# Optimization experiments

Measured on AMD Instinct MI355X. Metric: run time of the kernel, lower is better.

## Reference

```python
import jax, jax.numpy as jnp
import numpy as np

N = 100000
NFEAT = 128
NHID = 128
NCLASS = 40
E = 1600000
EPS = 1e-5


def _spmm(vals, src, dst, x, n):
    # y[dst] += vals * x[src]  (sparse adj @ x)
    return jax.ops.segment_sum(vals[:, None] * x[src], dst, num_segments=n)


def _bn(h, gamma, beta, rmean, rvar):
    # BatchNorm1d in eval mode (running statistics)
    return (h - rmean) * jax.lax.rsqrt(rvar + EPS) * gamma + beta


def setup_inputs() -> dict:
    key = jax.random.key(0)
    ks = jax.random.split(key, 24)
    inp = {
        'x': jax.random.normal(ks[0], (N, NFEAT), dtype=jnp.float32),
        'M': jax.random.uniform(ks[1], (N, 1), dtype=jnp.float32),
        'AM': jax.random.uniform(ks[2], (N, 1), dtype=jnp.float32),
        'srcZ': jax.random.randint(ks[3], (E,), 0, N, dtype=jnp.int32),
        'dstZ': jax.random.randint(ks[4], (E,), 0, N, dtype=jnp.int32),
        'valsZ': jax.random.uniform(ks[5], (E,), dtype=jnp.float32),
        'src': jax.random.randint(ks[6], (E,), 0, N, dtype=jnp.int32),
        'dst': jax.random.randint(ks[7], (E,), 0, N, dtype=jnp.int32),
        'vals': jax.random.uniform(ks[8], (E,), dtype=jnp.float32),
        # layer 0 (PaGConv) params
        'W0': jax.random.normal(ks[9], (NHID, NFEAT), dtype=jnp.float32) * (1.414 / np.sqrt(NFEAT)),
        'b0': jnp.zeros((NHID,), dtype=jnp.float32),
        'g0': jnp.ones((NHID,), dtype=jnp.float32),
        'be0': jnp.zeros((NHID,), dtype=jnp.float32),
        'rm0': jax.random.normal(ks[10], (NHID,), dtype=jnp.float32) * 0.1,
        'rv0': jax.random.uniform(ks[11], (NHID,), dtype=jnp.float32) + 0.5,
        # layer 1 (GConv) params
        'W1': jax.random.normal(ks[12], (NHID, NHID), dtype=jnp.float32) * (1.414 / np.sqrt(NHID)),
        'b1': jnp.zeros((NHID,), dtype=jnp.float32),
        'g1': jnp.ones((NHID,), dtype=jnp.float32),
        'be1': jnp.zeros((NHID,), dtype=jnp.float32),
        'rm1': jax.random.normal(ks[13], (NHID,), dtype=jnp.float32) * 0.1,
        'rv1': jax.random.uniform(ks[14], (NHID,), dtype=jnp.float32) + 0.5,
        # layer 2 (GConv) params
        'W2': jax.random.normal(ks[15], (NCLASS, NHID), dtype=jnp.float32) * (1.414 / np.sqrt(NHID)),
        'b2': jnp.zeros((NCLASS,), dtype=jnp.float32),
    }
    return inp


def reference(x, M, AM, srcZ, dstZ, valsZ, src, dst, vals,
              W0, b0, g0, be0, rm0, rv0,
              W1, b1, g1, be1, rm1, rv1,
              W2, b2):
    n = x.shape[0]
    # layer 0: PaGConv with adjZ: fc(spmm(adjZ, M*x) * AM), then BN + ReLU (dropout off in eval)
    h = _spmm(valsZ, srcZ, dstZ, M * x, n) * AM
    h = h @ W0.T + b0
    h = jax.nn.relu(_bn(h, g0, be0, rm0, rv0))
    # layer 1: GConv with adj: fc(spmm(adj, h)), then BN + ReLU
    h = _spmm(vals, src, dst, h, n)
    h = h @ W1.T + b1
    h = jax.nn.relu(_bn(h, g1, be1, rm1, rv1))
    # layer 2: GConv, then log_softmax
    h = _spmm(vals, src, dst, h, n)
    h = h @ W2.T + b2
    return jax.nn.log_softmax(h, axis=-1)
```

## Files before the change

kernel.cpp:

```cpp
#include <hip/hip_runtime.h>
#include <math.h>

#define NFEAT 128
#define NCLS 40
#define NCLSP 64
#define BINROWS 64
#define NBINMAX 1600
#define NBLKC 256
#define CHUNKMAX 6400
#define SEGC 7
#define RSMAX 2048

typedef short bf16x8 __attribute__((ext_vector_type(8)));
typedef float f32x4 __attribute__((ext_vector_type(4)));

__device__ __forceinline__ float bf2f(unsigned int lo16) {
  return __uint_as_float((lo16 & 0xffffu) << 16);
}
__device__ __forceinline__ unsigned int f2bf(float x) {
  unsigned int u = __float_as_uint(x);
  return (u + 0x7fffu + ((u >> 16) & 1u)) >> 16;
}

__global__ __launch_bounds__(256) void prep_all(
    const float* b0, const float* g0, const float* be0,
    const float* rm0, const float* rv0,
    const float* b1, const float* g1, const float* be1,
    const float* rm1, const float* rv1,
    float* sc0, float* sh0, float* sc1, float* sh1,
    const float* __restrict__ W0, const float* __restrict__ W1,
    const float* __restrict__ W2,
    unsigned short* __restrict__ Wb0, unsigned short* __restrict__ Wb1,
    unsigned short* __restrict__ W2hi, unsigned short* __restrict__ W2lo,
    const float* __restrict__ x, const float* __restrict__ Mv,
    unsigned short* __restrict__ xm, int n) {
  int t = threadIdx.x;
  if (blockIdx.x == 0) {
    if (t < 128) {
      float s = g0[t] * rsqrtf(rv0[t] + 1e-5f);
      sc0[t] = s;
      sh0[t] = (b0[t] - rm0[t]) * s + be0[t];
    } else {
      int i = t - 128;
      float s = g1[i] * rsqrtf(rv1[i] + 1e-5f);
      sc1[i] = s;
      sh1[i] = (b1[i] - rm1[i]) * s + be1[i];
    }
    return;
  }
  if (blockIdx.x <= 20) {
    int i = (blockIdx.x - 1) * 256 + t;
    if (i < 4096) {
      const float* W = (i < 2048) ? W0 : W1;
      unsigned short* Wb = (i < 2048) ? Wb0 : Wb1;
      int j = (i < 2048) ? i : i - 2048;
      const float4* p = (const float4*)(W + (size_t)j * 8);
      float4 v0 = p[0], v1 = p[1];
      unsigned int o0 = f2bf(v0.x) | (f2bf(v0.y) << 16);
      unsigned int o1 = f2bf(v0.z) | (f2bf(v0.w) << 16);
      unsigned int o2 = f2bf(v1.x) | (f2bf(v1.y) << 16);
      unsigned int o3 = f2bf(v1.z) | (f2bf(v1.w) << 16);
      ((uint4*)Wb)[j] = make_uint4(o0, o1, o2, o3);
    } else {
      int j = i - 4096;
      int r = j >> 4;
      float v[8] = {0.f, 0.f, 0.f, 0.f, 0.f, 0.f, 0.f, 0.f};
      if (r < NCLS) {
        const float4* p = (const float4*)(W2 + (size_t)j * 8);
        float4 a = p[0], b = p[1];
        v[0] = a.x; v[1] = a.y; v[2] = a.z; v[3] = a.w;
        v[4] = b.x; v[5] = b.y; v[6] = b.z; v[7] = b.w;
      }
      unsigned int h[8], l[8];
#pragma unroll
      for (int q = 0; q < 8; ++q) {
        h[q] = f2bf(v[q]);
        l[q] = f2bf(v[q] - bf2f(h[q]));
      }
      ((uint4*)W2hi)[j] = make_uint4(h[0] | (h[1] << 16), h[2] | (h[3] << 16),
                                     h[4] | (h[5] << 16), h[6] | (h[7] << 16));
      ((uint4*)W2lo)[j] = make_uint4(l[0] | (l[1] << 16), l[2] | (l[3] << 16),
                                     l[4] | (l[5] << 16), l[6] | (l[7] << 16));
    }
    return;
  }
  int i = (blockIdx.x - 21) * 256 + t;
  if (i >= n * (NFEAT / 8)) return;
  int row = i >> 4;
  float m = Mv[row];
  const float4* p = (const float4*)(x + (size_t)i * 8);
  float4 v0 = p[0], v1 = p[1];
  unsigned int o0 = f2bf(v0.x * m) | (f2bf(v0.y * m) << 16);
  unsigned int o1 = f2bf(v0.z * m) | (f2bf(v0.w * m) << 16);
  unsigned int o2 = f2bf(v1.x * m) | (f2bf(v1.y * m) << 16);
  unsigned int o3 = f2bf(v1.z * m) | (f2bf(v1.w * m) << 16);
  ((uint4*)xm)[i] = make_uint4(o0, o1, o2, o3);
}

__global__ __launch_bounds__(256) void bin_sort2(
    const int* __restrict__ srcZ, const int* __restrict__ dstZ, const float* __restrict__ valZ,
    const int* __restrict__ srcA, const int* __restrict__ dstA, const float* __restrict__ valA,
    int2* __restrict__ DrmZ, int2* __restrict__ DrmA,
    int2* __restrict__ binsCZ, int2* __restrict__ binsCA,
    int E, int nbin, int chunk) {
  __shared__ int2 stage[CHUNKMAX];
  __shared__ int cur[NBINMAX];
  __shared__ int ps[256];
  const int t = threadIdx.x;
  int k = blockIdx.x;
  const int* srcp; const int* dstp; const float* valp; int2* Drm; int2* binsC;
  if (k < NBLKC) {
    srcp = srcZ; dstp = dstZ; valp = valZ; Drm = DrmZ; binsC = binsCZ;
  } else {
    k -= NBLKC;
    srcp = srcA; dstp = dstA; valp = valA; Drm = DrmA; binsC = binsCA;
  }
  for (int i = t; i < nbin; i += 256) cur[i] = 0;
  __syncthreads();
  const int e0 = k * chunk, e1 = min(E, e0 + chunk);
#pragma unroll 4
  for (int e = e0 + t; e < e1; e += 256) atomicAdd(&cur[dstp[e] >> 6], 1);
  __syncthreads();
  int loc[SEGC], cnt[SEGC];
  int s = 0;
#pragma unroll
  for (int j = 0; j < SEGC; ++j) {
    int i = t * SEGC + j;
    int v = (i < nbin) ? cur[i] : 0;
    loc[j] = s; cnt[j] = v;
    s += v;
  }
  ps[t] = s;
  __syncthreads();
  for (int o = 1; o < 256; o <<= 1) {
    int x = (t >= o) ? ps[t - o] : 0;
    __syncthreads();
    ps[t] += x;
    __syncthreads();
  }
  int ex = ps[t] - s;
#pragma unroll
  for (int j = 0; j < SEGC; ++j) {
    int i = t * SEGC + j;
    if (i < nbin) {
      int o = ex + loc[j];
      Drm[(size_t)k * nbin + i] = make_int2(e0 + o, cnt[j]);
      cur[i] = o;
    }
  }
  __syncthreads();
#pragma unroll 2
  for (int e = e0 + t; e < e1; e += 256) {
    int d = dstp[e];
    int p = atomicAdd(&cur[d >> 6], 1);
    stage[p] = make_int2(srcp[e] | ((d & 63) << 17), __float_as_int(valp[e]));
  }
  __syncthreads();
  const int n = e1 - e0;
  for (int i = t; i < n; i += 256) binsC[e0 + i] = stage[i];
}

__global__ __launch_bounds__(256) void transposeD2(
    const int2* __restrict__ DrmZ, const int2* __restrict__ DrmA,
    int2* __restrict__ DbmZ, int2* __restrict__ DbmA, int nbin, int tdb) {
  __shared__ int2 st[8][256];
  int t = threadIdx.x;
  int b = blockIdx.x;
  const int2* Drm; int2* Dbm;
  if (b < tdb) {
    Drm = DrmZ; Dbm = DbmZ;
  } else {
    b -= tdb;
    Drm = DrmA; Dbm = DbmA;
  }
  int i0 = b * 8;
#pragma unroll
  for (int j = 0; j < 8; ++j) {
    int i = i0 + j;
    st[j][t] = (i < nbin) ? Drm[(size_t)t * nbin + i] : make_int2(0, 0);
  }
  __syncthreads();
  {
    int j = t >> 5, ks = (t & 31) * 8;
    int i = i0 + j;
    if (i < nbin) {
      int2* q = &Dbm[(size_t)i * NBLKC + ks];
#pragma unroll
      for (int m = 0; m < 8; ++m) q[m] = st[j][ks + m];
    }
  }
}

__global__ __launch_bounds__(256) void row_sort2(
    const int2* __restrict__ DbmZ, const int2* __restrict__ DbmA,
    const int2* __restrict__ binsCZ, const int2* __restrict__ binsCA,
    int2* __restrict__ bins2Z, int2* __restrict__ bins2A,
    int2* __restrict__ rdZ, int2* __restrict__ rdA, int n, int nbin) {
  __shared__ int2 stage[RSMAX];
  __shared__ int ps[256];
  __shared__ int rcnt[BINROWS];
  __shared__ int roff[BINROWS];
  int b = blockIdx.x;
  const int t = threadIdx.x;
  const int2* Dbm; const int2* binsC; int2* bins2; int2* rowdesc;
  if (b < nbin) {
    Dbm = DbmZ; binsC = binsCZ; bins2 = bins2Z; rowdesc = rdZ;
  } else {
    b -= nbin;
    Dbm = DbmA; binsC = binsCA; bins2 = bins2A; rowdesc = rdA;
  }
  if (t < BINROWS) rcnt[t] = 0;
  int2 run = Dbm[(size_t)b * NBLKC + t];
  ps[t] = run.y;
  __syncthreads();
  for (int o = 1; o < 256; o <<= 1) {
    int x = (t >= o) ? ps[t - o] : 0;
    __syncthreads();
    ps[t] += x;
    __syncthreads();
  }
  int mystart = ps[t] - run.y;
  for (int j = 0; j < run.y; ++j) {
    int2 en = binsC[run.x + j];
    int idx = mystart + j;
    if (idx < RSMAX) stage[idx] = en;
    atomicAdd(&rcnt[(en.x >> 17) & 63], 1);
  }
  __syncthreads();
  const int bs = b * RSMAX;
  if (t < BINROWS) {
    int c = rcnt[t];
    int s = c;
#pragma unroll
    for (int o = 1; o < 64; o <<= 1) {
      int v = __shfl_up(s, o);
      if (t >= o) s += v;
    }
    int excl = s - c;
    int row = b * BINROWS + t;
    if (row < n) rowdesc[row] = make_int2(bs + excl, c);
    roff[t] = excl;
  }
  __syncthreads();
  int total = min(ps[255], RSMAX);
  for (int i = t; i < total; i += 256) {
    int2 en = stage[i];
    int row = (en.x >> 17) & 63;
    int p = atomicAdd(&roff[row], 1);
    bins2[bs + p] = en;
  }
}

template <bool SCALE>
__global__ __launch_bounds__(256) void spmm128_sorted(
    const int2* __restrict__ rowdesc, const int2* __restrict__ bins2,
    const unsigned short* __restrict__ X, const float* __restrict__ AM,
    unsigned short* __restrict__ Y, int n) {
  int row = (blockIdx.x * 256 + threadIdx.x) >> 6;
  int lane = threadIdx.x & 63;
  if (row >= n) return;
  int2 rd = rowdesc[row];
  int s = rd.x, d = rd.y;
  int half = lane >> 5, l32 = lane & 31;
  float s0 = 0.f, s1 = 0.f, s2 = 0.f, s3 = 0.f;
  for (int kb = 0; kb < d; kb += 64) {
    int rem = min(64, d - kb);
    int2 my = (lane < rem) ? bins2[s + kb + lane] : make_int2(0, 0);
    int myc = my.x & 0x1FFFF;
    float myw = __int_as_float(my.y);
    for (int k = 0; k < rem; k += 8) {
#pragma unroll
      for (int st = 0; st < 4; ++st) {
        int idx = k + 2 * st + half;
        int c = __shfl(myc, idx);
        float wv = __shfl(myw, idx);
        uint2 pv = *(const uint2*)(X + (size_t)c * NFEAT + l32 * 4);
        s0 += wv * bf2f(pv.x);
        s1 += wv * bf2f(pv.x >> 16);
        s2 += wv * bf2f(pv.y);
        s3 += wv * bf2f(pv.y >> 16);
      }
    }
  }
  s0 += __shfl_xor(s0, 32); s1 += __shfl_xor(s1, 32);
  s2 += __shfl_xor(s2, 32); s3 += __shfl_xor(s3, 32);
  if (SCALE) {
    float am = AM[row];
    s0 *= am; s1 *= am; s2 *= am; s3 *= am;
  }
  unsigned int pk = half ? (f2bf(s2) | (f2bf(s3) << 16)) : (f2bf(s0) | (f2bf(s1) << 16));
  ((unsigned int*)Y)[(size_t)row * (NFEAT / 2) + l32 * 2 + half] = pk;
}

template <bool FUSE_G2>
__global__ __launch_bounds__(256) void gemm_mfma128(
    const unsigned short* __restrict__ Y, const unsigned short* __restrict__ Wb,
    const float* __restrict__ scale, const float* __restrict__ shift,
    unsigned short* __restrict__ Out,
    const unsigned short* __restrict__ Whi, const unsigned short* __restrict__ Wlo,
    unsigned short* __restrict__ G2, int M) {
  const int wave = threadIdx.x >> 6;
  const int lane = threadIdx.x & 63;
  const int quad = lane >> 4;
  const int l16 = lane & 15;
  const int arow = blockIdx.x * 64 + wave * 16 + l16;
  const bool rv = arow < M;

  f32x4 acc[8];
#pragma unroll
  for (int c = 0; c < 8; ++c) acc[c] = (f32x4){0.f, 0.f, 0.f, 0.f};

#pragma unroll
  for (int kc = 0; kc < 128; kc += 32) {
    bf16x8 a = rv ? *(const bf16x8*)(Y + (size_t)arow * 128 + kc + quad * 8)
                  : (bf16x8){0, 0, 0, 0, 0, 0, 0, 0};
#pragma unroll
    for (int c = 0; c < 8; ++c) {
      bf16x8 b = *(const bf16x8*)(Wb + (size_t)(c * 16 + l16) * 128 + kc + quad * 8);
      acc[c] = __builtin_amdgcn_mfma_f32_16x16x32_bf16(a, b, acc[c], 0, 0, 0);
    }
  }

  const int orow0 = blockIdx.x * 64 + wave * 16 + quad * 4;

  if constexpr (!FUSE_G2) {
#pragma unroll
    for (int c = 0; c < 8; ++c) {
      int col = c * 16 + l16;
      float sc = scale[col], sh = shift[col];
#pragma unroll
      for (int r = 0; r < 4; ++r) {
        int orow = orow0 + r;
        if (orow < M) {
          float v = fmaxf(acc[c][r] * sc + sh, 0.f);
          Out[(size_t)orow * 128 + col] = (unsigned short)f2bf(v);
        }
      }
    }
  } else {
    __shared__ unsigned short Ht[64][136];
    const int lrow0 = wave * 16 + quad * 4;
#pragma unroll
    for (int c = 0; c < 8; ++c) {
      int col = c * 16 + l16;
      float sc = scale[col], sh = shift[col];
#pragma unroll
      for (int r = 0; r < 4; ++r) {
        float v = fmaxf(acc[c][r] * sc + sh, 0.f);
        Ht[lrow0 + r][col] = (unsigned short)f2bf(v);
      }
    }
    __syncthreads();
    bf16x8 af[4];
#pragma unroll
    for (int kc = 0; kc < 4; ++kc)
      af[kc] = *(const bf16x8*)(&Ht[wave * 16 + l16][kc * 32 + quad * 8]);
    f32x4 acc2[4];
#pragma unroll
    for (int c2 = 0; c2 < 4; ++c2) acc2[c2] = (f32x4){0.f, 0.f, 0.f, 0.f};
#pragma unroll
    for (int kc = 0; kc < 4; ++kc) {
#pragma unroll
      for (int c2 = 0; c2 < 4; ++c2) {
        bf16x8 bh = *(const bf16x8*)(Whi + (size_t)(c2 * 16 + l16) * 128 + kc * 32 + quad * 8);
        bf16x8 bl = *(const bf16x8*)(Wlo + (size_t)(c2 * 16 + l16) * 128 + kc * 32 + quad * 8);
        acc2[c2] = __builtin_amdgcn_mfma_f32_16x16x32_bf16(af[kc], bh, acc2[c2], 0, 0, 0);
        acc2[c2] = __builtin_amdgcn_mfma_f32_16x16x32_bf16(af[kc], bl, acc2[c2], 0, 0, 0);
      }
    }
#pragma unroll
    for (int c2 = 0; c2 < 4; ++c2) {
      int col = c2 * 16 + l16;
#pragma unroll
      for (int r = 0; r < 4; ++r) {
        int orow = orow0 + r;
        if (orow < M) G2[(size_t)orow * NCLSP + col] = (unsigned short)f2bf(acc2[c2][r]);
      }
    }
  }
}

__global__ __launch_bounds__(256) void spmm_softmax64(
    const int2* __restrict__ rowdesc, const int2* __restrict__ bins2,
    const unsigned short* __restrict__ G2, const float* __restrict__ b2,
    float* __restrict__ out, int n) {
  int row = (blockIdx.x * 256 + threadIdx.x) >> 6;
  int lane = threadIdx.x & 63;
  if (row >= n) return;
  const int eidx = lane >> 4, q = lane & 15;
  const bool vq = q < (NCLS / 4);
  float4 bv = vq ? *(const float4*)(b2 + q * 4) : make_float4(0.f, 0.f, 0.f, 0.f);

  int2 rdv = rowdesc[row];
  int s0i = rdv.x, d = rdv.y;
  float a0 = 0.f, a1 = 0.f, a2 = 0.f, a3 = 0.f;
  for (int kb = 0; kb < d; kb += 64) {
    int rem = min(64, d - kb);
    int2 my = (lane < rem) ? bins2[s0i + kb + lane] : make_int2(0, 0);
    int myc = my.x & 0x1FFFF;
    float myw = __int_as_float(my.y);
    int steps = (rem + 3) >> 2;
#pragma unroll 4
    for (int st = 0; st < steps; ++st) {
      int idx = st * 4 + eidx;
      int c = __shfl(myc, idx);
      float wv = __shfl(myw, idx);
      uint2 pv = *(const uint2*)(G2 + (size_t)c * NCLSP + q * 4);
      a0 += wv * bf2f(pv.x);
      a1 += wv * bf2f(pv.x >> 16);
      a2 += wv * bf2f(pv.y);
      a3 += wv * bf2f(pv.y >> 16);
    }
  }
  a0 += __shfl_xor(a0, 16); a1 += __shfl_xor(a1, 16);
  a2 += __shfl_xor(a2, 16); a3 += __shfl_xor(a3, 16);
  a0 += __shfl_xor(a0, 32); a1 += __shfl_xor(a1, 32);
  a2 += __shfl_xor(a2, 32); a3 += __shfl_xor(a3, 32);
  float z0 = a0 + bv.x, z1 = a1 + bv.y, z2 = a2 + bv.z, z3 = a3 + bv.w;
  bool par = (eidx == 0) && vq;
  float m = par ? fmaxf(fmaxf(z0, z1), fmaxf(z2, z3)) : -INFINITY;
#pragma unroll
  for (int o = 1; o < 64; o <<= 1) m = fmaxf(m, __shfl_xor(m, o));
  float ex = par ? (__expf(z0 - m) + __expf(z1 - m) + __expf(z2 - m) + __expf(z3 - m)) : 0.f;
#pragma unroll
  for (int o = 1; o < 64; o <<= 1) ex += __shfl_xor(ex, o);
  float lg = m + __logf(ex);
  if (par) {
    *(float4*)&out[(size_t)row * NCLS + q * 4] =
        make_float4(z0 - lg, z1 - lg, z2 - lg, z3 - lg);
  }
}


extern "C" void kernel_launch(void* const* d_in, const int* in_sizes, int n_in,
                              void* d_out, int out_size, void* d_ws, size_t ws_size,
                              hipStream_t stream) {
  const float* x    = (const float*)d_in[0];
  const float* Mv   = (const float*)d_in[1];
  const float* AM   = (const float*)d_in[2];
  const int* srcZ   = (const int*)d_in[3];
  const int* dstZ   = (const int*)d_in[4];
  const float* valsZ= (const float*)d_in[5];
  const int* src    = (const int*)d_in[6];
  const int* dst    = (const int*)d_in[7];
  const float* vals = (const float*)d_in[8];
  const float* W0   = (const float*)d_in[9];
  const float* b0   = (const float*)d_in[10];
  const float* g0   = (const float*)d_in[11];
  const float* be0  = (const float*)d_in[12];
  const float* rm0  = (const float*)d_in[13];
  const float* rv0  = (const float*)d_in[14];
  const float* W1   = (const float*)d_in[15];
  const float* b1   = (const float*)d_in[16];
  const float* g1   = (const float*)d_in[17];
  const float* be1  = (const float*)d_in[18];
  const float* rm1  = (const float*)d_in[19];
  const float* rv1  = (const float*)d_in[20];
  const float* W2   = (const float*)d_in[21];
  const float* b2   = (const float*)d_in[22];
  float* out = (float*)d_out;

  const int N = in_sizes[1];
  const int E = in_sizes[3];
  const int NBIN = (N + BINROWS - 1) / BINROWS;
  const int CHUNK = (E + NBLKC - 1) / NBLKC;

  char* w = (char*)d_ws;
  size_t off = 0;
  auto alloc = [&](size_t bytes) -> void* {
    void* p = w + off;
    off = (off + bytes + 255) & ~(size_t)255;
    return p;
  };
  const size_t bins2Bytes = (size_t)NBIN * RSMAX * 8;
  const size_t bufBytes = (size_t)N * NFEAT * 2;
  int2* binsCZ = (int2*)alloc((size_t)NBLKC * CHUNK * 8);
  int2* binsCA = (int2*)alloc((size_t)NBLKC * CHUNK * 8);
  int2* bins2A = (int2*)alloc(bins2Bytes);
  int2* rdZ = (int2*)alloc((size_t)N * 8);
  int2* rdA = (int2*)alloc((size_t)N * 8);
  unsigned short* xm = (unsigned short*)alloc(bufBytes);
  unsigned short* bufA = (unsigned short*)alloc(bufBytes);
  unsigned short* bufB = (unsigned short*)alloc(bins2Bytes > bufBytes ? bins2Bytes : bufBytes);
  float* sc0 = (float*)alloc(128 * 4);
  float* sh0 = (float*)alloc(128 * 4);
  float* sc1 = (float*)alloc(128 * 4);
  float* sh1 = (float*)alloc(128 * 4);
  unsigned short* Wb0 = (unsigned short*)alloc(128 * 128 * 2);
  unsigned short* Wb1 = (unsigned short*)alloc(128 * 128 * 2);
  unsigned short* W2hi = (unsigned short*)alloc(64 * 128 * 2);
  unsigned short* W2lo = (unsigned short*)alloc(64 * 128 * 2);
  const size_t drmBytes = (size_t)NBLKC * NBIN * 8;
  int2* DrmZ = (int2*)((char*)bufA + 0 * drmBytes);
  int2* DrmA = (int2*)((char*)bufA + 1 * drmBytes);
  int2* DbmZ = (int2*)((char*)bufA + 2 * drmBytes);
  int2* DbmA = (int2*)((char*)bufA + 3 * drmBytes);
  int2* bins2Z = (int2*)bufB;
  unsigned short* G2 = bufB;

  const int RB = (N + 3) / 4;
  const int GB64 = (N + 63) / 64;
  const int TDB = (NBIN + 7) / 8;
  const int CONVB = (N * (NFEAT / 8) + 255) / 256;

  prep_all<<<21 + CONVB, 256, 0, stream>>>(b0, g0, be0, rm0, rv0, b1, g1, be1, rm1, rv1,
                                           sc0, sh0, sc1, sh1, W0, W1, W2,
                                           Wb0, Wb1, W2hi, W2lo, x, Mv, xm, N);

  bin_sort2<<<2 * NBLKC, 256, 0, stream>>>(srcZ, dstZ, valsZ, src, dst, vals,
                                           DrmZ, DrmA, binsCZ, binsCA, E, NBIN, CHUNK);
  transposeD2<<<2 * TDB, 256, 0, stream>>>(DrmZ, DrmA, DbmZ, DbmA, NBIN, TDB);
  row_sort2<<<2 * NBIN, 256, 0, stream>>>(DbmZ, DbmA, binsCZ, binsCA,
                                          bins2Z, bins2A, rdZ, rdA, N, NBIN);

  spmm128_sorted<true><<<RB, 256, 0, stream>>>(rdZ, bins2Z, xm, AM, bufA, N);
  gemm_mfma128<false><<<GB64, 256, 0, stream>>>(bufA, Wb0, sc0, sh0, bufB,
                                                nullptr, nullptr, nullptr, N);

  spmm128_sorted<false><<<RB, 256, 0, stream>>>(rdA, bins2A, bufB,
                                                (const float*)nullptr, bufA, N);
  gemm_mfma128<true><<<GB64, 256, 0, stream>>>(bufA, Wb1, sc1, sh1, nullptr,
                                               W2hi, W2lo, G2, N);

  spmm_softmax64<<<RB, 256, 0, stream>>>(rdA, bins2A, G2, b2, out, N);
}
```

Baseline: 510.8 us.

## Fuse sparse aggregation with the dense MFMA GEMM per layer

The separate SpMM and GEMM kernels for layers 0 and 1 are merged into one kernel. Each wave gathers 16 rows serially into a shared-memory tile and then runs the MFMA GEMM on that tile directly. This removes the write and re-read of the N×128 bf16 intermediate in global memory, along with two kernel launches. The cost is fewer waves in total, and each wave walks its rows one after another, which may reduce the memory-level parallelism of the latency-bound gather. The G2 output buffer is moved to the freed xm buffer.

Result: slower. 533.1 us (+4.4%).

```diff
diff --git a/kernel.cpp b/kernel.cpp
--- a/kernel.cpp
+++ b/kernel.cpp
@@ -251,79 +251,73 @@
   }
 }
 
-template <bool SCALE>
-__global__ __launch_bounds__(256) void spmm128_sorted(
+template <bool LAYER0>
+__global__ __launch_bounds__(128) void spmm_gemm128(
     const int2* __restrict__ rowdesc, const int2* __restrict__ bins2,
     const unsigned short* __restrict__ X, const float* __restrict__ AM,
-    unsigned short* __restrict__ Y, int n) {
-  int row = (blockIdx.x * 256 + threadIdx.x) >> 6;
-  int lane = threadIdx.x & 63;
-  if (row >= n) return;
-  int2 rd = rowdesc[row];
-  int s = rd.x, d = rd.y;
-  int half = lane >> 5, l32 = lane & 31;
-  float s0 = 0.f, s1 = 0.f, s2 = 0.f, s3 = 0.f;
-  for (int kb = 0; kb < d; kb += 64) {
-    int rem = min(64, d - kb);
-    int2 my = (lane < rem) ? bins2[s + kb + lane] : make_int2(0, 0);
-    int myc = my.x & 0x1FFFF;
-    float myw = __int_as_float(my.y);
-    for (int k = 0; k < rem; k += 8) {
-#pragma unroll
-      for (int st = 0; st < 4; ++st) {
-        int idx = k + 2 * st + half;
-        int c = __shfl(myc, idx);
-        float wv = __shfl(myw, idx);
-        uint2 pv = *(const uint2*)(X + (size_t)c * NFEAT + l32 * 4);
-        s0 += wv * bf2f(pv.x);
-        s1 += wv * bf2f(pv.x >> 16);
-        s2 += wv * bf2f(pv.y);
-        s3 += wv * bf2f(pv.y >> 16);
-      }
-    }
-  }
-  s0 += __shfl_xor(s0, 32); s1 += __shfl_xor(s1, 32);
-  s2 += __shfl_xor(s2, 32); s3 += __shfl_xor(s3, 32);
-  if (SCALE) {
-    float am = AM[row];
-    s0 *= am; s1 *= am; s2 *= am; s3 *= am;
-  }
-  unsigned int pk = half ? (f2bf(s2) | (f2bf(s3) << 16)) : (f2bf(s0) | (f2bf(s1) << 16));
-  ((unsigned int*)Y)[(size_t)row * (NFEAT / 2) + l32 * 2 + half] = pk;
-}
-
-template <bool FUSE_G2>
-__global__ __launch_bounds__(256) void gemm_mfma128(
-    const unsigned short* __restrict__ Y, const unsigned short* __restrict__ Wb,
+    const unsigned short* __restrict__ Wb,
     const float* __restrict__ scale, const float* __restrict__ shift,
-    unsigned short* __restrict__ Out,
     const unsigned short* __restrict__ Whi, const unsigned short* __restrict__ Wlo,
-    unsigned short* __restrict__ G2, int M) {
+    unsigned short* __restrict__ Out, int n) {
+  __shared__ unsigned short Yt[32][136];
   const int wave = threadIdx.x >> 6;
   const int lane = threadIdx.x & 63;
-  const int quad = lane >> 4;
-  const int l16 = lane & 15;
-  const int arow = blockIdx.x * 64 + wave * 16 + l16;
-  const bool rv = arow < M;
-
+  const int half = lane >> 5, l32 = lane & 31;
+  const int r0 = blockIdx.x * 32 + wave * 16;
+
+#pragma unroll 1
+  for (int j = 0; j < 16; ++j) {
+    int row = r0 + j;
+    float s0 = 0.f, s1 = 0.f, s2 = 0.f, s3 = 0.f;
+    if (row < n) {
+      int2 rd = rowdesc[row];
+      int s = rd.x, d = rd.y;
+      for (int kb = 0; kb < d; kb += 64) {
+        int rem = min(64, d - kb);
+        int2 my = (lane < rem) ? bins2[s + kb + lane] : make_int2(0, 0);
+        int myc = my.x & 0x1FFFF;
+        float myw = __int_as_float(my.y);
+        for (int k = 0; k < rem; k += 8) {
+#pragma unroll
+          for (int st = 0; st < 4; ++st) {
+            int idx = k + 2 * st + half;
+            int c = __shfl(myc, idx);
+            float wv = __shfl(myw, idx);
+            uint2 pv = *(const uint2*)(X + (size_t)c * NFEAT + l32 * 4);
+            s0 += wv * bf2f(pv.x);
+            s1 += wv * bf2f(pv.x >> 16);
+            s2 += wv * bf2f(pv.y);
+            s3 += wv * bf2f(pv.y >> 16);
+          }
+        }
+      }
+      s0 += __shfl_xor(s0, 32); s1 += __shfl_xor(s1, 32);
+      s2 += __shfl_xor(s2, 32); s3 += __shfl_xor(s3, 32);
+      if (LAYER0) {
+        float am = AM[row];
+        s0 *= am; s1 *= am; s2 *= am; s3 *= am;
+      }
+    }
+    unsigned int pk = half ? (f2bf(s2) | (f2bf(s3) << 16)) : (f2bf(s0) | (f2bf(s1) << 16));
+    *(unsigned int*)&Yt[wave * 16 + j][(l32 * 2 + half) * 2] = pk;
+  }
+
+  const int quad = lane >> 4, l16 = lane & 15;
+  const int orow0 = r0 + quad * 4;
   f32x4 acc[8];
 #pragma unroll
   for (int c = 0; c < 8; ++c) acc[c] = (f32x4){0.f, 0.f, 0.f, 0.f};
-
-#pragma unroll
-  for (int kc = 0; kc < 128; kc += 32) {
-    bf16x8 a = rv ? *(const bf16x8*)(Y + (size_t)arow * 128 + kc + quad * 8)
-                  : (bf16x8){0, 0, 0, 0, 0, 0, 0, 0};
+#pragma unroll
+  for (int kc = 0; kc < 4; ++kc) {
+    bf16x8 a = *(const bf16x8*)&Yt[wave * 16 + l16][kc * 32 + quad * 8];
 #pragma unroll
     for (int c = 0; c < 8; ++c) {
-      bf16x8 b = *(const bf16x8*)(Wb + (size_t)(c * 16 + l16) * 128 + kc + quad * 8);
+      bf16x8 b = *(const bf16x8*)(Wb + (size_t)(c * 16 + l16) * 128 + kc * 32 + quad * 8);
       acc[c] = __builtin_amdgcn_mfma_f32_16x16x32_bf16(a, b, acc[c], 0, 0, 0);
     }
   }
 
-  const int orow0 = blockIdx.x * 64 + wave * 16 + quad * 4;
-
-  if constexpr (!FUSE_G2) {
+  if constexpr (LAYER0) {
 #pragma unroll
     for (int c = 0; c < 8; ++c) {
       int col = c * 16 + l16;
@@ -331,15 +325,13 @@
 #pragma unroll
       for (int r = 0; r < 4; ++r) {
         int orow = orow0 + r;
-        if (orow < M) {
+        if (orow < n) {
           float v = fmaxf(acc[c][r] * sc + sh, 0.f);
           Out[(size_t)orow * 128 + col] = (unsigned short)f2bf(v);
         }
       }
     }
   } else {
-    __shared__ unsigned short Ht[64][136];
-    const int lrow0 = wave * 16 + quad * 4;
 #pragma unroll
     for (int c = 0; c < 8; ++c) {
       int col = c * 16 + l16;
@@ -347,25 +339,21 @@
 #pragma unroll
       for (int r = 0; r < 4; ++r) {
         float v = fmaxf(acc[c][r] * sc + sh, 0.f);
-        Ht[lrow0 + r][col] = (unsigned short)f2bf(v);
-      }
-    }
-    __syncthreads();
-    bf16x8 af[4];
-#pragma unroll
-    for (int kc = 0; kc < 4; ++kc)
-      af[kc] = *(const bf16x8*)(&Ht[wave * 16 + l16][kc * 32 + quad * 8]);
+        Yt[wave * 16 + quad * 4 + r][col] = (unsigned short)f2bf(v);
+      }
+    }
     f32x4 acc2[4];
 #pragma unroll
     for (int c2 = 0; c2 < 4; ++c2) acc2[c2] = (f32x4){0.f, 0.f, 0.f, 0.f};
 #pragma unroll
     for (int kc = 0; kc < 4; ++kc) {
+      bf16x8 hf = *(const bf16x8*)&Yt[wave * 16 + l16][kc * 32 + quad * 8];
 #pragma unroll
       for (int c2 = 0; c2 < 4; ++c2) {
         bf16x8 bh = *(const bf16x8*)(Whi + (size_t)(c2 * 16 + l16) * 128 + kc * 32 + quad * 8);
         bf16x8 bl = *(const bf16x8*)(Wlo + (size_t)(c2 * 16 + l16) * 128 + kc * 32 + quad * 8);
-        acc2[c2] = __builtin_amdgcn_mfma_f32_16x16x32_bf16(af[kc], bh, acc2[c2], 0, 0, 0);
-        acc2[c2] = __builtin_amdgcn_mfma_f32_16x16x32_bf16(af[kc], bl, acc2[c2], 0, 0, 0);
+        acc2[c2] = __builtin_amdgcn_mfma_f32_16x16x32_bf16(hf, bh, acc2[c2], 0, 0, 0);
+        acc2[c2] = __builtin_amdgcn_mfma_f32_16x16x32_bf16(hf, bl, acc2[c2], 0, 0, 0);
       }
     }
 #pragma unroll
@@ -374,7 +362,7 @@
 #pragma unroll
       for (int r = 0; r < 4; ++r) {
         int orow = orow0 + r;
-        if (orow < M) G2[(size_t)orow * NCLSP + col] = (unsigned short)f2bf(acc2[c2][r]);
+        if (orow < n) Out[(size_t)orow * NCLSP + col] = (unsigned short)f2bf(acc2[c2][r]);
       }
     }
   }
@@ -496,10 +484,10 @@
   int2* DbmZ = (int2*)((char*)bufA + 2 * drmBytes);
   int2* DbmA = (int2*)((char*)bufA + 3 * drmBytes);
   int2* bins2Z = (int2*)bufB;
-  unsigned short* G2 = bufB;
+  unsigned short* G2 = xm;
 
   const int RB = (N + 3) / 4;
-  const int GB64 = (N + 63) / 64;
+  const int MB32 = (N + 31) / 32;
   const int TDB = (NBIN + 7) / 8;
   const int CONVB = (N * (NFEAT / 8) + 255) / 256;
 
@@ -513,14 +501,11 @@
   row_sort2<<<2 * NBIN, 256, 0, stream>>>(DbmZ, DbmA, binsCZ, binsCA,
                                           bins2Z, bins2A, rdZ, rdA, N, NBIN);
 
-  spmm128_sorted<true><<<RB, 256, 0, stream>>>(rdZ, bins2Z, xm, AM, bufA, N);
-  gemm_mfma128<false><<<GB64, 256, 0, stream>>>(bufA, Wb0, sc0, sh0, bufB,
-                                                nullptr, nullptr, nullptr, N);
-
-  spmm128_sorted<false><<<RB, 256, 0, stream>>>(rdA, bins2A, bufB,
-                                                (const float*)nullptr, bufA, N);
-  gemm_mfma128<true><<<GB64, 256, 0, stream>>>(bufA, Wb1, sc1, sh1, nullptr,
-                                               W2hi, W2lo, G2, N);
+  spmm_gemm128<true><<<MB32, 128, 0, stream>>>(rdZ, bins2Z, xm, AM, Wb0, sc0, sh0,
+                                               nullptr, nullptr, bufA, N);
+
+  spmm_gemm128<false><<<MB32, 128, 0, stream>>>(rdA, bins2A, bufA, nullptr, Wb1, sc1, sh1,
+                                                W2hi, W2lo, G2, N);
 
   spmm_softmax64<<<RB, 256, 0, stream>>>(rdA, bins2A, G2, b2, out, N);
 }
```
